# Kernel optimization log

Measured on AMD Instinct MI355X. Metric: run time of the kernel, lower is better.

## Reference

```python
import jax, jax.numpy as jnp
import numpy as np
import math

D_MODEL = 512
EXPAND = 2
D_INNER = EXPAND * D_MODEL          # 1024
HEADDIM = 16
NHEADS = D_INNER // HEADDIM         # 64
NGROUPS = 1
D_STATE = 16
D_CONV = 4
CHUNK = 256
CONV_DIM = D_INNER + 2 * NGROUPS * D_STATE      # 1056
D_IN_PROJ = 2 * D_INNER + 2 * NGROUPS * D_STATE + NHEADS  # 2144
EPS = 1e-5


def setup_inputs() -> dict:
    key = jax.random.key(0)
    ks = jax.random.split(key, 9)
    B, L = 2, 4096
    u = jax.random.normal(ks[0], (B, L, D_MODEL), dtype=jnp.float32)
    in_proj_w = jax.random.normal(ks[1], (D_IN_PROJ, D_MODEL), dtype=jnp.float32) * (1.0 / math.sqrt(D_MODEL))
    conv_w = jax.random.normal(ks[2], (CONV_DIM, D_CONV), dtype=jnp.float32) * (1.0 / math.sqrt(D_CONV))
    conv_b = jnp.zeros((CONV_DIM,), dtype=jnp.float32)
    # dt_bias = inverse-softplus of dt sampled log-uniform in [1e-3, 1e-1]
    dt = jnp.exp(jax.random.uniform(ks[3], (NHEADS,)) * (math.log(0.1) - math.log(0.001)) + math.log(0.001))
    dt_bias = dt + jnp.log(-jnp.expm1(-dt))
    A_log = jnp.log(jax.random.uniform(ks[4], (NHEADS,), minval=1.0, maxval=16.0))
    D_skip = jnp.ones((NHEADS,), dtype=jnp.float32)
    norm_w = jnp.ones((D_INNER,), dtype=jnp.float32)
    out_proj_w = jax.random.normal(ks[5], (D_MODEL, D_INNER), dtype=jnp.float32) * (1.0 / math.sqrt(D_INNER))
    return {"u": u, "in_proj_w": in_proj_w, "conv_w": conv_w, "conv_b": conv_b,
            "dt_bias": dt_bias, "A_log": A_log, "D_skip": D_skip,
            "norm_w": norm_w, "out_proj_w": out_proj_w}


def _segsum(x):
    # x: (..., T) -> (..., T, T) lower-triangular cumulative segment sums
    T = x.shape[-1]
    cs = jnp.cumsum(x, axis=-1)
    s = cs[..., :, None] - cs[..., None, :]
    mask = jnp.tril(jnp.ones((T, T), dtype=bool))
    return jnp.where(mask, s, -jnp.inf)


def _ssd(xdt, dA, Bm, Cm):
    # xdt: (b,l,h,p) already multiplied by dt; dA: (b,l,h); Bm,Cm: (b,l,h,n)
    b, l, h, p = xdt.shape
    n = Bm.shape[-1]
    nc = l // CHUNK
    xr = xdt.reshape(b, nc, CHUNK, h, p)
    Br = Bm.reshape(b, nc, CHUNK, h, n)
    Cr = Cm.reshape(b, nc, CHUNK, h, n)
    dAr = dA.reshape(b, nc, CHUNK, h).transpose(0, 3, 1, 2)  # (b,h,nc,c)
    A_cs = jnp.cumsum(dAr, axis=-1)
    # intra-chunk (diagonal blocks)
    Ldec = jnp.exp(_segsum(dAr))                              # (b,h,nc,c,c)
    Y_diag = jnp.einsum('bclhn,bcshn,bhcls,bcshp->bclhp', Cr, Br, Ldec, xr)
    # per-chunk final states
    decay_states = jnp.exp(A_cs[..., -1:] - A_cs)             # (b,h,nc,c)
    states = jnp.einsum('bclhn,bhcl,bclhp->bchpn', Br, decay_states, xr)
    states = jnp.concatenate([jnp.zeros_like(states[:, :1]), states], axis=1)
    chunk_sums = jnp.pad(A_cs[..., -1], ((0, 0), (0, 0), (1, 0)))  # (b,h,nc+1)
    decay_chunk = jnp.exp(_segsum(chunk_sums))                # (b,h,nc+1,nc+1)
    new_states = jnp.einsum('bhzc,bchpn->bzhpn', decay_chunk, states)
    prev_states = new_states[:, :-1]                          # (b,nc,h,p,n)
    # inter-chunk contribution
    state_decay_out = jnp.exp(A_cs)                           # (b,h,nc,c)
    Y_off = jnp.einsum('bclhn,bchpn,bhcl->bclhp', Cr, prev_states, state_decay_out)
    return (Y_diag + Y_off).reshape(b, l, h, p)


def _forward(u, in_proj_w, conv_w, conv_b, dt_bias, A_log, D_skip, norm_w, out_proj_w):
    b, l, _ = u.shape
    zxbcdt = jnp.einsum('bld,ed->ble', u, in_proj_w)
    z = zxbcdt[..., :D_INNER]
    xBC = zxbcdt[..., D_INNER:D_INNER + CONV_DIM]
    dt = zxbcdt[..., D_INNER + CONV_DIM:]
    dt = jax.nn.softplus(dt + dt_bias)                        # (b,l,h)
    # causal depthwise conv1d + silu
    xBC_t = xBC.transpose(0, 2, 1)                            # (b, conv_dim, l)
    conv_out = jax.lax.conv_general_dilated(
        xBC_t, conv_w[:, None, :], window_strides=(1,),
        padding=[(D_CONV - 1, 0)], feature_group_count=CONV_DIM,
        dimension_numbers=('NCH', 'OIH', 'NCH'))
    xBC = jax.nn.silu((conv_out + conv_b[None, :, None]).transpose(0, 2, 1))
    x = xBC[..., :D_INNER].reshape(b, l, NHEADS, HEADDIM)
    Bg = xBC[..., D_INNER:D_INNER + NGROUPS * D_STATE].reshape(b, l, NGROUPS, D_STATE)
    Cg = xBC[..., D_INNER + NGROUPS * D_STATE:].reshape(b, l, NGROUPS, D_STATE)
    hpg = NHEADS // NGROUPS
    Bm = jnp.repeat(Bg, hpg, axis=2)                          # (b,l,h,n)
    Cm = jnp.repeat(Cg, hpg, axis=2)
    A = -jnp.exp(A_log)                                       # (h,)
    dA = dt * A                                               # (b,l,h)
    y = _ssd(x * dt[..., None], dA, Bm, Cm)
    y = y + x * D_skip[None, None, :, None]
    y = y.reshape(b, l, D_INNER)
    # gated RMSNorm (norm_before_gate=False): norm(y * silu(z)) * w
    y = y * jax.nn.silu(z)
    y = y * jax.lax.rsqrt(jnp.mean(y * y, axis=-1, keepdims=True) + EPS) * norm_w
    return jnp.einsum('ble,de->bld', y, out_proj_w)


def reference(u, in_proj_w, conv_w, conv_b, dt_bias, A_log, D_skip, norm_w, out_proj_w):
    return _forward(u, in_proj_w, conv_w, conv_b, dt_bias, A_log, D_skip, norm_w, out_proj_w)
```

## Files before the change

kernel.cpp:

```cpp
#include <hip/hip_runtime.h>
#include <hip/hip_bf16.h>
#include <math.h>

#define D_MODEL   512
#define D_INNER   1024
#define NHEADS    64
#define HEADDIM   16
#define D_STATE   16
#define CONV_DIM  1056
#define D_IN_PROJ 2144
#define CHUNK     256
#define NCHUNK    16
#define BATCH     2
#define SEQ       4096
#define ROWS      (BATCH * SEQ)
#define LDZX      2176

typedef __bf16    bf16x8 __attribute__((ext_vector_type(8)));
typedef _Float16  f16x8  __attribute__((ext_vector_type(8)));
typedef float     f32x4  __attribute__((ext_vector_type(4)));
typedef float     f32x16 __attribute__((ext_vector_type(16)));
typedef unsigned short u16x8 __attribute__((ext_vector_type(8)));
typedef unsigned int   u32x4 __attribute__((ext_vector_type(4)));

__device__ __forceinline__ float softplusf(float x) {
    return (x > 20.f) ? x : log1pf(expf(x));
}
__device__ __forceinline__ float siluf(float x) {
    return x / (1.f + expf(-x));
}
__device__ __forceinline__ unsigned short f2b(float x) {
    union { __hip_bfloat16 h; unsigned short u; } cv;
    cv.h = __float2bfloat16(x);
    return cv.u;
}
__device__ __forceinline__ float b2f(unsigned short u) {
    union { float f; unsigned int i; } c;
    c.i = (unsigned int)u << 16;
    return c.f;
}
__device__ __forceinline__ void load_lds16(const unsigned short* g, unsigned short* l) {
    __builtin_amdgcn_global_load_lds(
        (const __attribute__((address_space(1))) void*)g,
        (__attribute__((address_space(3))) void*)l,
        16, 0, 0);
}

__global__ __launch_bounds__(256) void cast8(const float* __restrict__ in,
                                             unsigned short* __restrict__ out, int n) {
    int i = (blockIdx.x * blockDim.x + threadIdx.x) * 8;
    if (i >= n) return;
    float4 a = *(const float4*)(in + i);
    float4 b = *(const float4*)(in + i + 4);
    u16x8 o;
    o[0] = f2b(a.x); o[1] = f2b(a.y); o[2] = f2b(a.z); o[3] = f2b(a.w);
    o[4] = f2b(b.x); o[5] = f2b(b.y); o[6] = f2b(b.z); o[7] = f2b(b.w);
    *(u16x8*)(out + i) = o;
}

__global__ __launch_bounds__(256) void castpad8(const float* __restrict__ in,
                                                unsigned short* __restrict__ out,
                                                int n, int npad) {
    int i = (blockIdx.x * blockDim.x + threadIdx.x) * 8;
    if (i >= npad) return;
    u16x8 o;
    if (i + 8 <= n) {
        float4 a = *(const float4*)(in + i);
        float4 b = *(const float4*)(in + i + 4);
        o[0] = f2b(a.x); o[1] = f2b(a.y); o[2] = f2b(a.z); o[3] = f2b(a.w);
        o[4] = f2b(b.x); o[5] = f2b(b.y); o[6] = f2b(b.z); o[7] = f2b(b.w);
    } else {
        #pragma unroll
        for (int j = 0; j < 8; ++j) o[j] = (i + j < n) ? f2b(in[i + j]) : (unsigned short)0;
    }
    *(u16x8*)(out + i) = o;
}

__global__ __launch_bounds__(256) void gemm_in(const unsigned short* __restrict__ A,
                                               const unsigned short* __restrict__ B,
                                               unsigned short* __restrict__ C16,
                                               float* __restrict__ dtsp,
                                               const float* __restrict__ dtb) {
    __shared__ unsigned short smem[16384];
    const int t    = threadIdx.x;
    const int wave = t >> 6;
    const int lane = t & 63;
    const int bid  = blockIdx.x;
    const int swz  = (bid & 7) * 136 + (bid >> 3);
    const int by   = swz / 17;
    const int bx   = swz - by * 17;
    const int bm   = by * 128;
    const int bn   = bx * 128;
    const int wr   = wave >> 1;
    const int wc   = wave & 1;

    const int srow = wave * 16 + (lane >> 2);
    const int scol = (lane & 3) * 8;
    const unsigned short* ga0 = A + (size_t)(bm + srow) * 512 + scol;
    const unsigned short* ga1 = A + (size_t)(bm + 64 + srow) * 512 + scol;
    const unsigned short* gb0 = B + (size_t)(bn + srow) * 512 + scol;
    const unsigned short* gb1 = B + (size_t)(bn + 64 + srow) * 512 + scol;

    const int fr = lane & 15;
    const int kb = (lane >> 4) * 8;

    f32x4 acc[4][4] = {};

    load_lds16(ga0, smem + wave * 512);
    load_lds16(ga1, smem + 2048 + wave * 512);
    load_lds16(gb0, smem + 8192 + wave * 512);
    load_lds16(gb1, smem + 8192 + 2048 + wave * 512);
    __syncthreads();

    int cur = 0;
    for (int it = 0; it < 16; ++it) {
        if (it + 1 < 16) {
            const int k0 = (it + 1) * 32;
            const int nb = cur ^ 1;
            load_lds16(ga0 + k0, smem + nb * 4096 + wave * 512);
            load_lds16(ga1 + k0, smem + nb * 4096 + 2048 + wave * 512);
            load_lds16(gb0 + k0, smem + 8192 + nb * 4096 + wave * 512);
            load_lds16(gb1 + k0, smem + 8192 + nb * 4096 + 2048 + wave * 512);
        }
        const unsigned short* Ab = smem + cur * 4096;
        const unsigned short* Bb = smem + 8192 + cur * 4096;
        bf16x8 af[4], bfr[4];
        #pragma unroll
        for (int m = 0; m < 4; ++m)
            af[m] = *reinterpret_cast<const bf16x8*>(&Ab[(wr * 64 + m * 16 + fr) * 32 + kb]);
        #pragma unroll
        for (int n = 0; n < 4; ++n)
            bfr[n] = *reinterpret_cast<const bf16x8*>(&Bb[(wc * 64 + n * 16 + fr) * 32 + kb]);
        #pragma unroll
        for (int m = 0; m < 4; ++m)
            #pragma unroll
            for (int n = 0; n < 4; ++n)
                acc[m][n] = __builtin_amdgcn_mfma_f32_16x16x32_bf16(af[m], bfr[n], acc[m][n], 0, 0, 0);
        __syncthreads();
        cur ^= 1;
    }

    if (bn == 2048) {
        #pragma unroll
        for (int m = 0; m < 4; ++m) {
            #pragma unroll
            for (int n = 0; n < 4; ++n) {
                const int col = bn + wc * 64 + fr + n * 16;
                if (col >= 2080 && col < 2144) {
                    const int h = col - 2080;
                    const float bias = dtb[h];
                    #pragma unroll
                    for (int j = 0; j < 4; ++j) {
                        const int row = bm + wr * 64 + ((lane >> 4) << 2) + m * 16 + j;
                        dtsp[(size_t)row * 64 + h] = softplusf(acc[m][n][j] + bias);
                    }
                }
            }
        }
    }
    const int cr0 = bm + wr * 64 + ((lane >> 4) << 2);
    const int cc0 = bn + wc * 64 + fr;
    #pragma unroll
    for (int m = 0; m < 4; ++m)
        #pragma unroll
        for (int n = 0; n < 4; ++n)
            #pragma unroll
            for (int j = 0; j < 4; ++j)
                C16[(size_t)(cr0 + m * 16 + j) * LDZX + cc0 + n * 16] = f2b(acc[m][n][j]);
}

__global__ __launch_bounds__(256) void gemm_out(const unsigned short* __restrict__ A,
                                                const unsigned short* __restrict__ B,
                                                float* __restrict__ C) {
    __shared__ unsigned short smem[12288];
    const int t    = threadIdx.x;
    const int wave = t >> 6;
    const int lane = t & 63;
    const int bid  = blockIdx.x;
    const int swz  = (bid & 7) * 64 + (bid >> 3);
    const int by   = swz >> 3;
    const int bx   = swz & 7;
    const int bm   = by * 128;
    const int bn   = bx * 64;
    const int wr   = wave >> 1;
    const int wc   = wave & 1;

    const int srow = wave * 16 + (lane >> 2);
    const int scol = (lane & 3) * 8;
    const unsigned short* ga0 = A + (size_t)(bm + srow) * 1024 + scol;
    const unsigned short* ga1 = A + (size_t)(bm + 64 + srow) * 1024 + scol;
    const unsigned short* gb0 = B + (size_t)(bn + srow) * 1024 + scol;

    const int fr = lane & 15;
    const int kb = (lane >> 4) * 8;

    f32x4 acc[4][2] = {};

    load_lds16(ga0, smem + wave * 512);
    load_lds16(ga1, smem + 2048 + wave * 512);
    load_lds16(gb0, smem + 8192 + wave * 512);
    __syncthreads();

    int cur = 0;
    for (int it = 0; it < 32; ++it) {
        if (it + 1 < 32) {
            const int k0 = (it + 1) * 32;
            const int nb = cur ^ 1;
            load_lds16(ga0 + k0, smem + nb * 4096 + wave * 512);
            load_lds16(ga1 + k0, smem + nb * 4096 + 2048 + wave * 512);
            load_lds16(gb0 + k0, smem + 8192 + nb * 2048 + wave * 512);
        }
        const unsigned short* Ab = smem + cur * 4096;
        const unsigned short* Bb = smem + 8192 + cur * 2048;
        bf16x8 af[4], bfr[2];
        #pragma unroll
        for (int m = 0; m < 4; ++m)
            af[m] = *reinterpret_cast<const bf16x8*>(&Ab[(wr * 64 + m * 16 + fr) * 32 + kb]);
        #pragma unroll
        for (int n = 0; n < 2; ++n)
            bfr[n] = *reinterpret_cast<const bf16x8*>(&Bb[(wc * 32 + n * 16 + fr) * 32 + kb]);
        #pragma unroll
        for (int m = 0; m < 4; ++m)
            #pragma unroll
            for (int n = 0; n < 2; ++n)
                acc[m][n] = __builtin_amdgcn_mfma_f32_16x16x32_bf16(af[m], bfr[n], acc[m][n], 0, 0, 0);
        __syncthreads();
        cur ^= 1;
    }

    const int cr0 = bm + wr * 64 + ((lane >> 4) << 2);
    const int cc0 = bn + wc * 32 + fr;
    #pragma unroll
    for (int m = 0; m < 4; ++m)
        #pragma unroll
        for (int n = 0; n < 2; ++n)
            #pragma unroll
            for (int j = 0; j < 4; ++j)
                C[(size_t)(cr0 + m * 16 + j) * 512 + cc0 + n * 16] = acc[m][n][j];
}

__global__ void conv_silu44(const unsigned short* __restrict__ zxb, const float* __restrict__ cw,
                            const float* __restrict__ cb, unsigned short* __restrict__ xcb) {
    int idx = blockIdx.x * blockDim.x + threadIdx.x;
    if (idx >= (ROWS / 4) * (CONV_DIM / 4)) return;
    const int cq  = idx % (CONV_DIM / 4);
    const int blq = idx / (CONV_DIM / 4);
    const int bl0 = blq * 4;
    const int l0  = bl0 % SEQ;
    const int c4  = cq * 4;
    const unsigned short* base = zxb + (size_t)bl0 * LDZX + D_INNER + c4;
    float4 w0 = *(const float4*)(cw + (c4 + 0) * 4);
    float4 w1 = *(const float4*)(cw + (c4 + 1) * 4);
    float4 w2 = *(const float4*)(cw + (c4 + 2) * 4);
    float4 w3 = *(const float4*)(cw + (c4 + 3) * 4);
    float4 bb = *(const float4*)(cb + c4);
    float4 in[7];
    #pragma unroll
    for (int k = 0; k < 7; ++k) {
        const int off = k - 3;
        if (l0 == 0 && k < 3) {
            in[k] = make_float4(0.f, 0.f, 0.f, 0.f);
        } else {
            ushort4 uu = *(const ushort4*)(base + (long)off * LDZX);
            in[k] = make_float4(b2f(uu.x), b2f(uu.y), b2f(uu.z), b2f(uu.w));
        }
    }
    #pragma unroll
    for (int r = 0; r < 4; ++r) {
        ushort4 o;
        o.x = f2b(siluf(bb.x + w0.x * in[r].x + w0.y * in[r + 1].x + w0.z * in[r + 2].x + w0.w * in[r + 3].x));
        o.y = f2b(siluf(bb.y + w1.x * in[r].y + w1.y * in[r + 1].y + w1.z * in[r + 2].y + w1.w * in[r + 3].y));
        o.z = f2b(siluf(bb.z + w2.x * in[r].z + w2.y * in[r + 1].z + w2.z * in[r + 2].z + w2.w * in[r + 3].z));
        o.w = f2b(siluf(bb.w + w3.x * in[r].w + w3.y * in[r + 1].w + w3.z * in[r + 2].w + w3.w * in[r + 3].w));
        *(ushort4*)(xcb + (size_t)(bl0 + r) * CONV_DIM + c4) = o;
    }
}

__global__ __launch_bounds__(256, 3) void ssd_chunk(const unsigned short* __restrict__ xcb,
                                                    const float* __restrict__ dtsp,
                                                    const float* __restrict__ A_log,
                                                    unsigned short* __restrict__ ypre16,
                                                    float* __restrict__ states,
                                                    float* __restrict__ csb,
                                                    float* __restrict__ csum) {
    __shared__ _Float16 Bb[256][16];
    __shared__ _Float16 Cb[256][16];
    __shared__ _Float16 Xt[16][264];
    __shared__ _Float16 Xdt[16][264];
    __shared__ _Float16 Bt[16][264];
    __shared__ float csL[256];
    __shared__ float wsumL[4];
    __shared__ float stpart[4][16][16];

    const int bid = blockIdx.x;
    const int h = bid & 63;
    const int c = (bid >> 6) & 15;
    const int b = bid >> 10;
    const int t = threadIdx.x;
    const int wv = t >> 6;
    const int lane = t & 63;
    const int fr = lane & 15;
    const int hi = lane >> 4;
    const int l31 = lane & 31;
    const int hi5 = lane >> 5;
    const int row = b * SEQ + c * CHUNK + t;

    float Ah  = -__expf(A_log[h]);
    float dtv = dtsp[(size_t)row * NHEADS + h];
    float val = dtv * Ah;
    #pragma unroll
    for (int off = 1; off < 64; off <<= 1) {
        float o = __shfl_up(val, off, 64);
        if (lane >= off) val += o;
    }
    if (lane == 63) wsumL[wv] = val;
    __syncthreads();
    float pre = 0.f, cl = 0.f;
    #pragma unroll
    for (int w2 = 0; w2 < 4; ++w2) {
        float s = wsumL[w2];
        if (w2 < wv) pre += s;
        cl += s;
    }
    float cst = val + pre;
    csL[t] = cst;
    csb[(size_t)bid * 256 + t] = cst;
    if (t == 0) csum[(b * 64 + h) * 16 + c] = cl;
    float dec_t = __expf(cl - cst);

    const unsigned short* xrow = xcb + (size_t)row * CONV_DIM;
    u16x8 braw0 = *(const u16x8*)(xrow + D_INNER);
    u16x8 braw1 = *(const u16x8*)(xrow + D_INNER + 8);
    u16x8 craw0 = *(const u16x8*)(xrow + D_INNER + D_STATE);
    u16x8 craw1 = *(const u16x8*)(xrow + D_INNER + D_STATE + 8);
    u16x8 xraw0 = *(const u16x8*)(xrow + h * HEADDIM);
    u16x8 xraw1 = *(const u16x8*)(xrow + h * HEADDIM + 8);
    float bv[16], cv[16], xv[16];
    #pragma unroll
    for (int n = 0; n < 8; ++n) {
        bv[n] = b2f(braw0[n]); bv[8 + n] = b2f(braw1[n]);
        cv[n] = b2f(craw0[n]); cv[8 + n] = b2f(craw1[n]);
        xv[n] = b2f(xraw0[n]); xv[8 + n] = b2f(xraw1[n]);
    }
    {
        f16x8 pk;
        #pragma unroll
        for (int n = 0; n < 8; ++n) pk[n] = (_Float16)cv[n];
        *(f16x8*)&Cb[t][0] = pk;
        #pragma unroll
        for (int n = 0; n < 8; ++n) pk[n] = (_Float16)cv[8 + n];
        *(f16x8*)&Cb[t][8] = pk;
        #pragma unroll
        for (int n = 0; n < 8; ++n) pk[n] = (_Float16)bv[n];
        *(f16x8*)&Bb[t][0] = pk;
        #pragma unroll
        for (int n = 0; n < 8; ++n) pk[n] = (_Float16)bv[8 + n];
        *(f16x8*)&Bb[t][8] = pk;
    }
    #pragma unroll
    for (int n = 0; n < 16; ++n) {
        Bt[n][t] = (_Float16)bv[n];
        float xd = xv[n] * dtv;
        Xt[n][t] = (_Float16)xd;
        Xdt[n][t] = (_Float16)(xd * dec_t);
    }
    __syncthreads();

    const int browbase = b * SEQ + c * CHUNK;
    const f32x16 z16 = {};

    #pragma unroll
    for (int halfi = 0; halfi < 2; ++halfi) {
        const int rt = (halfi == 0) ? wv : 7 - wv;
        const int t0 = rt * 32;
        const float cs_t = csL[t0 + l31];
        const f16x8 cfrag = *(const f16x8*)&Cb[t0 + l31][hi5 * 8];
        f32x16 yacc = {};
        for (int sb = 0; sb <= rt; ++sb) {
            const int s0 = sb * 32;
            f16x8 bfrag = *(const f16x8*)&Bb[s0 + l31][hi5 * 8];
            f32x16 sp = __builtin_amdgcn_mfma_f32_32x32x16_f16(bfrag, cfrag, z16, 0, 0, 0);
            const bool diag = (sb == rt);
            unsigned int D[8];
            #pragma unroll
            for (int j = 0; j < 8; ++j) {
                const int q0 = 2 * j;
                const int sr0 = (q0 & 3) + 8 * (q0 >> 2) + 4 * hi5;
                float p0 = sp[q0] * __expf(cs_t - csL[s0 + sr0]);
                float p1 = sp[q0 + 1] * __expf(cs_t - csL[s0 + sr0 + 1]);
                if (diag) {
                    p0 = (sr0 <= l31) ? p0 : 0.f;
                    p1 = (sr0 + 1 <= l31) ? p1 : 0.f;
                }
                D[j] = __builtin_bit_cast(unsigned int, __builtin_amdgcn_cvt_pkrtz(p0, p1));
            }
            unsigned int pD[8];
            #pragma unroll
            for (int j = 0; j < 8; ++j) pD[j] = (unsigned int)__shfl_xor((int)D[j], 32, 64);
            u32x4 fa;
            fa[0] = hi5 ? pD[2] : D[0];
            fa[1] = hi5 ? pD[3] : D[1];
            fa[2] = hi5 ? D[2] : pD[0];
            fa[3] = hi5 ? D[3] : pD[1];
            f16x8 pf0 = __builtin_bit_cast(f16x8, fa);
            f16x8 xf0 = *(const f16x8*)&Xt[fr][s0 + hi5 * 8];
            yacc = __builtin_amdgcn_mfma_f32_32x32x16_f16(pf0, xf0, yacc, 0, 0, 0);
            fa[0] = hi5 ? pD[6] : D[4];
            fa[1] = hi5 ? pD[7] : D[5];
            fa[2] = hi5 ? D[6] : pD[4];
            fa[3] = hi5 ? D[7] : pD[5];
            f16x8 pf1 = __builtin_bit_cast(f16x8, fa);
            f16x8 xf1 = *(const f16x8*)&Xt[fr][s0 + 16 + hi5 * 8];
            yacc = __builtin_amdgcn_mfma_f32_32x32x16_f16(pf1, xf1, yacc, 0, 0, 0);
        }
        if (l31 < 16) {
            #pragma unroll
            for (int q = 0; q < 16; ++q) {
                const int tr = t0 + (q & 3) + 8 * (q >> 2) + 4 * hi5;
                ypre16[(size_t)(browbase + tr) * D_INNER + h * HEADDIM + l31] = f2b(yacc[q]);
            }
        }
    }

    const int r0w = wv * 64;
    f32x4 stacc = {};
    #pragma unroll
    for (int kt = 0; kt < 2; ++kt) {
        f16x8 xa = *(const f16x8*)&Xdt[fr][r0w + kt * 32 + hi * 8];
        f16x8 bb2 = *(const f16x8*)&Bt[fr][r0w + kt * 32 + hi * 8];
        stacc = __builtin_amdgcn_mfma_f32_16x16x32_f16(xa, bb2, stacc, 0, 0, 0);
    }
    #pragma unroll
    for (int j = 0; j < 4; ++j)
        stpart[wv][hi * 4 + j][fr] = stacc[j];
    __syncthreads();
    {
        const int p = t >> 4, n = t & 15;
        float st = stpart[0][p][n] + stpart[1][p][n] + stpart[2][p][n] + stpart[3][p][n];
        states[(size_t)bid * 256 + t] = st;
    }
}

__global__ __launch_bounds__(256) void ssd_rec(const float* __restrict__ states,
                                               const float* __restrict__ csum,
                                               float* __restrict__ prevst) {
    __shared__ float dec[16];
    const int bh = blockIdx.x;
    const int b = bh >> 6, h = bh & 63;
    const int t = threadIdx.x;
    if (t < 16) dec[t] = __expf(csum[bh * 16 + t]);
    float sv[16];
    #pragma unroll
    for (int c = 0; c < NCHUNK; ++c)
        sv[c] = states[((size_t)((b * 16 + c) * 64 + h)) * 256 + t];
    __syncthreads();
    float run = 0.f;
    #pragma unroll
    for (int c = 0; c < NCHUNK; ++c) {
        prevst[((size_t)((b * 16 + c) * 64 + h)) * 256 + t] = run;
        run = run * dec[c] + sv[c];
    }
}

__global__ __launch_bounds__(512, 4) void ssd_off_norm(const unsigned short* __restrict__ xcb,
                                                       const unsigned short* __restrict__ zxb,
                                                       const unsigned short* __restrict__ ypre16,
                                                       const float* __restrict__ prevst,
                                                       const float* __restrict__ csb,
                                                       const float* __restrict__ Dskip,
                                                       const float* __restrict__ normw,
                                                       unsigned short* __restrict__ yout) {
    __shared__ float Cs[16][16];
    __shared__ float csS[64][16];
    __shared__ float nw[1024];
    __shared__ float Dn[64];
    __shared__ float red[16][8];

    const int blk = blockIdx.x;
    const int bc = blk >> 4;
    const int rb = blk & 15;
    const int r0 = rb * 16;
    const int b = bc >> 4, c = bc & 15;
    const int brow0 = b * SEQ + c * CHUNK;
    const int t = threadIdx.x;
    const int ch0 = t * 2;
    const int h = ch0 >> 4;
    const int p0 = ch0 & 15;
    const int wv = t >> 6;
    const int lane = t & 63;

    if (t < 256) *(float4*)&nw[t * 4] = *(const float4*)(normw + t * 4);
    else if (t < 320) Dn[t - 256] = Dskip[t - 256];
    if (t < 64) {
        int r = t >> 2, n4 = (t & 3) * 4;
        ushort4 uu = *(const ushort4*)(xcb + (size_t)(brow0 + r0 + r) * CONV_DIM
                                       + D_INNER + D_STATE + n4);
        Cs[r][n4 + 0] = b2f(uu.x); Cs[r][n4 + 1] = b2f(uu.y);
        Cs[r][n4 + 2] = b2f(uu.z); Cs[r][n4 + 3] = b2f(uu.w);
    }
    #pragma unroll
    for (int i = t; i < 1024; i += 512) {
        int r = i & 15, hh = i >> 4;
        csS[hh][r] = csb[(size_t)(bc * 64 + hh) * 256 + r0 + r];
    }

    float ps[2][16];
    {
        const float* pbase = prevst + (size_t)(bc * 64 + h) * 256 + p0 * 16;
        #pragma unroll
        for (int n4 = 0; n4 < 16; n4 += 4) {
            *(float4*)&ps[0][n4] = *(const float4*)(pbase + n4);
            *(float4*)&ps[1][n4] = *(const float4*)(pbase + 16 + n4);
        }
    }
    __syncthreads();

    const float d = Dn[h];
    const float nw0 = nw[ch0], nw1 = nw[ch0 + 1];

    for (int r = 0; r < 16; ++r) {
        const size_t grow = (size_t)(brow0 + r0 + r);
        ushort2 yu = *(const ushort2*)(ypre16 + grow * D_INNER + ch0);
        ushort2 xu = *(const ushort2*)(xcb + grow * CONV_DIM + ch0);
        ushort2 zu = *(const ushort2*)(zxb + grow * LDZX + ch0);
        float sdo = __expf(csS[h][r]);
        float off0 = 0.f, off1 = 0.f;
        #pragma unroll
        for (int n = 0; n < 16; ++n) {
            float cn = Cs[r][n];
            off0 += cn * ps[0][n];
            off1 += cn * ps[1][n];
        }
        float g0 = (b2f(yu.x) + sdo * off0 + b2f(xu.x) * d) * siluf(b2f(zu.x));
        float g1 = (b2f(yu.y) + sdo * off1 + b2f(xu.y) * d) * siluf(b2f(zu.y));
        float s = g0 * g0 + g1 * g1;
        #pragma unroll
        for (int o = 32; o > 0; o >>= 1) s += __shfl_down(s, o, 64);
        if (lane == 0) red[r][wv] = s;
        __syncthreads();
        float tot = 0.f;
        #pragma unroll
        for (int w2 = 0; w2 < 8; ++w2) tot += red[r][w2];
        float rstd = rsqrtf(tot * (1.f / (float)D_INNER) + 1e-5f);
        ushort2 o2;
        o2.x = f2b(g0 * rstd * nw0);
        o2.y = f2b(g1 * rstd * nw1);
        *(ushort2*)(yout + grow * D_INNER + ch0) = o2;
    }
}

extern "C" void kernel_launch(void* const* d_in, const int* in_sizes, int n_in,
                              void* d_out, int out_size, void* d_ws, size_t ws_size,
                              hipStream_t stream) {
    const float* u     = (const float*)d_in[0];
    const float* Win   = (const float*)d_in[1];
    const float* cw    = (const float*)d_in[2];
    const float* cb    = (const float*)d_in[3];
    const float* dtb   = (const float*)d_in[4];
    const float* Alog  = (const float*)d_in[5];
    const float* Dsk   = (const float*)d_in[6];
    const float* normw = (const float*)d_in[7];
    const float* Wout  = (const float*)d_in[8];
    float* out = (float*)d_out;

    float* ws = (float*)d_ws;
    unsigned short* zxb = (unsigned short*)ws;
    float* dtsp   = ws + 8912896;
    float* csb    = dtsp + 524288;
    float* st     = csb + 524288;
    float* pst    = st + 524288;
    float* csum   = pst + 524288;
    unsigned short* ypre16 = (unsigned short*)(csum + 2048);
    unsigned short* xcb    = (unsigned short*)((float*)ypre16 + 4194304);
    unsigned short* yn_bf  = (unsigned short*)((float*)xcb + 4325376);
    unsigned short* u_bf   = (unsigned short*)((float*)yn_bf + 2097152);
    unsigned short* win_bf  = (unsigned short*)((float*)u_bf + 2097152);
    unsigned short* wout_bf = (unsigned short*)((float*)win_bf + 557056);

    cast8<<<2048, 256, 0, stream>>>(u, u_bf, 4194304);
    castpad8<<<544, 256, 0, stream>>>(Win, win_bf, 2144 * 512, 2176 * 512);
    cast8<<<256, 256, 0, stream>>>(Wout, wout_bf, 524288);

    gemm_in<<<1088, 256, 0, stream>>>(u_bf, win_bf, zxb, dtsp, dtb);

    conv_silu44<<<(ROWS / 4) * (CONV_DIM / 4) / 256, 256, 0, stream>>>(zxb, cw, cb, xcb);
    ssd_chunk<<<BATCH * NCHUNK * NHEADS, 256, 0, stream>>>(xcb, dtsp, Alog, ypre16, st, csb, csum);
    ssd_rec<<<BATCH * NHEADS, 256, 0, stream>>>(st, csum, pst);
    ssd_off_norm<<<512, 512, 0, stream>>>(xcb, zxb, ypre16, pst, csb, Dsk, normw, yn_bf);

    gemm_out<<<512, 256, 0, stream>>>(yn_bf, wout_bf, out);
}
```

Before: 145.4 us.

## Triple-buffer GEMM LDS loads with vmcnt waits and single barrier per iteration

Both bf16 GEMMs move from double-buffered LDS with two __syncthreads per iteration to a three-stage ring that prefetches two K-tiles ahead. Each iteration waits with an explicit s_waitcnt vmcnt plus one s_barrier, and the next stage is issued after the fragment reads, so loads overlap the MFMAs. The block-index swizzle is dropped in favour of a plain 2D grid, which may lose L2 locality. LDS use grows, which can lower occupancy.

```diff
diff --git a/kernel.cpp b/kernel.cpp
--- a/kernel.cpp
+++ b/kernel.cpp
@@ -81,16 +81,13 @@
                                                unsigned short* __restrict__ C16,
                                                float* __restrict__ dtsp,
                                                const float* __restrict__ dtb) {
-    __shared__ unsigned short smem[16384];
+    __shared__ unsigned short As[12288];
+    __shared__ unsigned short Bs[12288];
     const int t    = threadIdx.x;
     const int wave = t >> 6;
     const int lane = t & 63;
-    const int bid  = blockIdx.x;
-    const int swz  = (bid & 7) * 136 + (bid >> 3);
-    const int by   = swz / 17;
-    const int bx   = swz - by * 17;
-    const int bm   = by * 128;
-    const int bn   = bx * 128;
+    const int bm   = blockIdx.y * 128;
+    const int bn   = blockIdx.x * 128;
     const int wr   = wave >> 1;
     const int wc   = wave & 1;
 
@@ -105,25 +102,25 @@
     const int kb = (lane >> 4) * 8;
 
     f32x4 acc[4][4] = {};
-
-    load_lds16(ga0, smem + wave * 512);
-    load_lds16(ga1, smem + 2048 + wave * 512);
-    load_lds16(gb0, smem + 8192 + wave * 512);
-    load_lds16(gb1, smem + 8192 + 2048 + wave * 512);
-    __syncthreads();
-
-    int cur = 0;
-    for (int it = 0; it < 16; ++it) {
-        if (it + 1 < 16) {
-            const int k0 = (it + 1) * 32;
-            const int nb = cur ^ 1;
-            load_lds16(ga0 + k0, smem + nb * 4096 + wave * 512);
-            load_lds16(ga1 + k0, smem + nb * 4096 + 2048 + wave * 512);
-            load_lds16(gb0 + k0, smem + 8192 + nb * 4096 + wave * 512);
-            load_lds16(gb1 + k0, smem + 8192 + nb * 4096 + 2048 + wave * 512);
-        }
-        const unsigned short* Ab = smem + cur * 4096;
-        const unsigned short* Bb = smem + 8192 + cur * 4096;
+    const int NIT = 16;
+
+    auto stage = [&](int it) {
+        const int k0 = it * 32;
+        const int bo = (it % 3) * 4096;
+        load_lds16(ga0 + k0, As + bo + wave * 512);
+        load_lds16(ga1 + k0, As + bo + 2048 + wave * 512);
+        load_lds16(gb0 + k0, Bs + bo + wave * 512);
+        load_lds16(gb1 + k0, Bs + bo + 2048 + wave * 512);
+    };
+    stage(0);
+    stage(1);
+
+    for (int it = 0; it < NIT; ++it) {
+        if (it < NIT - 1) asm volatile("s_waitcnt vmcnt(4)" ::: "memory");
+        else              asm volatile("s_waitcnt vmcnt(0)" ::: "memory");
+        __builtin_amdgcn_s_barrier();
+        const unsigned short* Ab = As + (it % 3) * 4096;
+        const unsigned short* Bb = Bs + (it % 3) * 4096;
         bf16x8 af[4], bfr[4];
         #pragma unroll
         for (int m = 0; m < 4; ++m)
@@ -131,13 +128,12 @@
         #pragma unroll
         for (int n = 0; n < 4; ++n)
             bfr[n] = *reinterpret_cast<const bf16x8*>(&Bb[(wc * 64 + n * 16 + fr) * 32 + kb]);
+        if (it + 2 < NIT) stage(it + 2);
         #pragma unroll
         for (int m = 0; m < 4; ++m)
             #pragma unroll
             for (int n = 0; n < 4; ++n)
                 acc[m][n] = __builtin_amdgcn_mfma_f32_16x16x32_bf16(af[m], bfr[n], acc[m][n], 0, 0, 0);
-        __syncthreads();
-        cur ^= 1;
     }
 
     if (bn == 2048) {
@@ -172,16 +168,13 @@
 __global__ __launch_bounds__(256) void gemm_out(const unsigned short* __restrict__ A,
                                                 const unsigned short* __restrict__ B,
                                                 float* __restrict__ C) {
-    __shared__ unsigned short smem[12288];
+    __shared__ unsigned short As[12288];
+    __shared__ unsigned short Bs[6144];
     const int t    = threadIdx.x;
     const int wave = t >> 6;
     const int lane = t & 63;
-    const int bid  = blockIdx.x;
-    const int swz  = (bid & 7) * 64 + (bid >> 3);
-    const int by   = swz >> 3;
-    const int bx   = swz & 7;
-    const int bm   = by * 128;
-    const int bn   = bx * 64;
+    const int bm   = blockIdx.y * 128;
+    const int bn   = blockIdx.x * 64;
     const int wr   = wave >> 1;
     const int wc   = wave & 1;
 
@@ -195,23 +188,23 @@
     const int kb = (lane >> 4) * 8;
 
     f32x4 acc[4][2] = {};
-
-    load_lds16(ga0, smem + wave * 512);
-    load_lds16(ga1, smem + 2048 + wave * 512);
-    load_lds16(gb0, smem + 8192 + wave * 512);
-    __syncthreads();
-
-    int cur = 0;
-    for (int it = 0; it < 32; ++it) {
-        if (it + 1 < 32) {
-            const int k0 = (it + 1) * 32;
-            const int nb = cur ^ 1;
-            load_lds16(ga0 + k0, smem + nb * 4096 + wave * 512);
-            load_lds16(ga1 + k0, smem + nb * 4096 + 2048 + wave * 512);
-            load_lds16(gb0 + k0, smem + 8192 + nb * 2048 + wave * 512);
-        }
-        const unsigned short* Ab = smem + cur * 4096;
-        const unsigned short* Bb = smem + 8192 + cur * 2048;
+    const int NIT = 32;
+
+    auto stage = [&](int it) {
+        const int k0 = it * 32;
+        load_lds16(ga0 + k0, As + (it % 3) * 4096 + wave * 512);
+        load_lds16(ga1 + k0, As + (it % 3) * 4096 + 2048 + wave * 512);
+        load_lds16(gb0 + k0, Bs + (it % 3) * 2048 + wave * 512);
+    };
+    stage(0);
+    stage(1);
+
+    for (int it = 0; it < NIT; ++it) {
+        if (it < NIT - 1) asm volatile("s_waitcnt vmcnt(3)" ::: "memory");
+        else              asm volatile("s_waitcnt vmcnt(0)" ::: "memory");
+        __builtin_amdgcn_s_barrier();
+        const unsigned short* Ab = As + (it % 3) * 4096;
+        const unsigned short* Bb = Bs + (it % 3) * 2048;
         bf16x8 af[4], bfr[2];
         #pragma unroll
         for (int m = 0; m < 4; ++m)
@@ -219,13 +212,12 @@
         #pragma unroll
         for (int n = 0; n < 2; ++n)
             bfr[n] = *reinterpret_cast<const bf16x8*>(&Bb[(wc * 32 + n * 16 + fr) * 32 + kb]);
+        if (it + 2 < NIT) stage(it + 2);
         #pragma unroll
         for (int m = 0; m < 4; ++m)
             #pragma unroll
             for (int n = 0; n < 2; ++n)
                 acc[m][n] = __builtin_amdgcn_mfma_f32_16x16x32_bf16(af[m], bfr[n], acc[m][n], 0, 0, 0);
-        __syncthreads();
-        cur ^= 1;
     }
 
     const int cr0 = bm + wr * 64 + ((lane >> 4) << 2);
@@ -581,12 +573,12 @@
     castpad8<<<544, 256, 0, stream>>>(Win, win_bf, 2144 * 512, 2176 * 512);
     cast8<<<256, 256, 0, stream>>>(Wout, wout_bf, 524288);
 
-    gemm_in<<<1088, 256, 0, stream>>>(u_bf, win_bf, zxb, dtsp, dtb);
+    gemm_in<<<dim3(17, 64), 256, 0, stream>>>(u_bf, win_bf, zxb, dtsp, dtb);
 
     conv_silu44<<<(ROWS / 4) * (CONV_DIM / 4) / 256, 256, 0, stream>>>(zxb, cw, cb, xcb);
     ssd_chunk<<<BATCH * NCHUNK * NHEADS, 256, 0, stream>>>(xcb, dtsp, Alog, ypre16, st, csb, csum);
     ssd_rec<<<BATCH * NHEADS, 256, 0, stream>>>(st, csum, pst);
     ssd_off_norm<<<512, 512, 0, stream>>>(xcb, zxb, ypre16, pst, csb, Dsk, normw, yn_bf);
 
-    gemm_out<<<512, 256, 0, stream>>>(yn_bf, wout_bf, out);
-}
+    gemm_out<<<dim3(8, 64), 256, 0, stream>>>(yn_bf, wout_bf, out);
+}
```

Result: slower. 151.4 us (+4.1%).
